# Performance work log

Hardware: AMD Instinct MI355X
Metric: run time of the kernel (lower is better)

## Reference

```python
import jax, jax.numpy as jnp
import numpy as np

MINC, MAXC, RATIO = 1, 16, 0.25


def _upsample2x(x):
    # bilinear, align_corners=False, (h,w) -> (2h,2w)
    B, C, h, w = x.shape
    def idx(n_in, n_out):
        src = (jnp.arange(n_out) + 0.5) * (n_in / n_out) - 0.5
        i0f = jnp.floor(src)
        t = (src - i0f).astype(jnp.float32)
        i0 = jnp.clip(i0f, 0, n_in - 1).astype(jnp.int32)
        i1 = jnp.clip(i0f + 1, 0, n_in - 1).astype(jnp.int32)
        return i0, i1, t
    i0, i1, t = idx(h, 2 * h)
    x = x[:, :, i0, :] * (1 - t)[None, None, :, None] + x[:, :, i1, :] * t[None, None, :, None]
    j0, j1, s = idx(w, 2 * w)
    x = x[:, :, :, j0] * (1 - s)[None, None, None, :] + x[:, :, :, j1] * s[None, None, None, :]
    return x


def _connection_counts(x):
    # DFDetector: down(0.5 bilinear, no antialias) == 2x2 avg-pool for even H,W
    B, C, H, W = x.shape
    xd = x.reshape(B, C, H // 2, 2, W // 2, 2).mean(axis=(3, 5))
    xu = _upsample2x(xd)
    df = jnp.abs(x - xu).sum(axis=1)  # [B,H,W]
    dmin = df.reshape(B, -1).min(axis=1)[:, None, None]
    dmax = df.reshape(B, -1).max(axis=1)[:, None, None]
    dn = (df - dmin) / (dmax - dmin + 1e-8)
    return (MINC + jnp.round(dn * (MAXC - MINC))).astype(jnp.int32)  # [B,H,W]


def setup_inputs() -> dict:
    key = jax.random.key(0)
    k0, k1, k2 = jax.random.split(key, 3)
    C = 64
    return {
        "x": jax.random.normal(k0, (2, C, 64, 64), jnp.float32),
        "ln_gamma": jnp.ones((C,), jnp.float32),
        "ln_beta": jnp.zeros((C,), jnp.float32),
        "w1": jax.random.normal(k1, (2 * C, C), jnp.float32) * 0.05,
        "b1": jnp.zeros((2 * C,), jnp.float32),
        "w2": jax.random.normal(k2, (C, 2 * C), jnp.float32) * 0.05,
        "b2": jnp.zeros((C,), jnp.float32),
    }


def reference(x, ln_gamma, ln_beta, w1, b1, w2, b2):
    B, C, H, W = x.shape
    k = _connection_counts(x).reshape(B, H * W)  # [B,HW] in [1,16]

    win = max(3, int(min(H, W) * RATIO))
    win += (win % 2 == 0)  # 17 for 64x64
    half = win // 2
    offs = np.arange(-half, half + 1)
    dy = np.repeat(offs, win); dx = np.tile(offs, win)             # [K2]
    py = np.repeat(np.arange(H), W); px = np.tile(np.arange(W), H)  # [HW]
    ny = py[:, None] + dy[None, :]; nx = px[:, None] + dx[None, :]
    valid = jnp.asarray((ny >= 0) & (ny < H) & (nx >= 0) & (nx < W))          # [HW,K2]
    idx = jnp.asarray(np.clip(ny, 0, H - 1) * W + np.clip(nx, 0, W - 1))      # [HW,K2]

    x_flat = x.transpose(0, 2, 3, 1).reshape(B, H * W, C)
    xn = x_flat / jnp.maximum(jnp.linalg.norm(x_flat, axis=-1, keepdims=True), 1e-12)

    nbr = xn[:, idx]                                   # [B,HW,K2,C]
    sim = jnp.einsum('bpc,bpkc->bpk', xn, nbr)         # cosine similarity
    sim = jnp.where(valid[None], sim, -1e30)           # mask out-of-bounds

    top_sim, top_i = jax.lax.top_k(sim, MAXC)          # [B,HW,16]
    mask = (jnp.arange(MAXC)[None, None, :] < k[:, :, None]).astype(x.dtype)
    wts = jnp.exp(top_sim) * mask
    wts = wts / wts.sum(-1, keepdims=True)

    gidx = jnp.take_along_axis(jnp.broadcast_to(idx[None], (B,) + idx.shape), top_i, axis=2)
    feats = jax.vmap(lambda xf, gi: xf[gi])(x_flat, gidx)  # [B,HW,16,C]
    agg = jnp.einsum('bpk,bpkc->bpc', wts, feats)
    out = agg.reshape(B, H, W, C).transpose(0, 3, 1, 2)

    # per-pixel channel LayerNorm (intent of nn.LayerNorm([C,1,1]))
    mu = x.mean(axis=1, keepdims=True)
    var = ((x - mu) ** 2).mean(axis=1, keepdims=True)
    xln = (x - mu) / jnp.sqrt(var + 1e-5) * ln_gamma[None, :, None, None] + ln_beta[None, :, None, None]

    enh = out + xln
    h1 = jax.nn.relu(jnp.einsum('bchw,dc->bdhw', enh, w1) + b1[None, :, None, None])
    ffn = jnp.einsum('bdhw,cd->bchw', h1, w2) + b2[None, :, None, None]
    return enh + ffn
```

## Files before the change

kernel.cpp:

```cpp
#include <hip/hip_runtime.h>
#include <math.h>

#define BB  2
#define CC  64
#define HH  64
#define WW  64
#define PP  4096
#define CHW 262144
#define KMAX 16
#define NSL 576

#define OFF_SIMS 0
#define OFF_XT   4718592
#define OFF_XNH  5242880
#define OFF_XNL  5505024
#define OFF_DF   5767168
#define OFF_PMN  5775360
#define OFF_PMX  5775616

typedef __bf16 bf16x8 __attribute__((ext_vector_type(8)));
typedef __bf16 bf16x4 __attribute__((ext_vector_type(4)));
typedef float  f32x4  __attribute__((ext_vector_type(4)));

#define DPP_STEP(v, ctrl, OP) { int _s = __builtin_amdgcn_update_dpp( \
    __float_as_int(v), __float_as_int(v), ctrl, 0xf, 0xf, false); \
    v = OP(v, __int_as_float(_s)); }
__device__ __forceinline__ float addf_(float a, float b) { return a + b; }
__device__ __forceinline__ float wave_max_b(float v) {
    DPP_STEP(v, 0x111, fmaxf) DPP_STEP(v, 0x112, fmaxf) DPP_STEP(v, 0x114, fmaxf)
    DPP_STEP(v, 0x118, fmaxf) DPP_STEP(v, 0x142, fmaxf) DPP_STEP(v, 0x143, fmaxf)
    return __int_as_float(__builtin_amdgcn_readlane(__float_as_int(v), 63));
}
__device__ __forceinline__ float wave_min_b(float v) {
    DPP_STEP(v, 0x111, fminf) DPP_STEP(v, 0x112, fminf) DPP_STEP(v, 0x114, fminf)
    DPP_STEP(v, 0x118, fminf) DPP_STEP(v, 0x142, fminf) DPP_STEP(v, 0x143, fminf)
    return __int_as_float(__builtin_amdgcn_readlane(__float_as_int(v), 63));
}
__device__ __forceinline__ float wave_sum_b(float v) {
    DPP_STEP(v, 0x111, addf_) DPP_STEP(v, 0x112, addf_) DPP_STEP(v, 0x114, addf_)
    DPP_STEP(v, 0x118, addf_) DPP_STEP(v, 0x142, addf_) DPP_STEP(v, 0x143, addf_)
    return __int_as_float(__builtin_amdgcn_readlane(__float_as_int(v), 63));
}

__global__ __launch_bounds__(256) void k_prep(const float* __restrict__ x,
        float* __restrict__ xt,
        unsigned short* __restrict__ xnh, unsigned short* __restrict__ xnl,
        float* __restrict__ df, float* __restrict__ pmn, float* __restrict__ pmx) {
    __shared__ float T[64*33];
    __shared__ float xds[2304];
    __shared__ float pdf[8*33], pss[8*33];
    __shared__ float sinv[32];
    int t = threadIdx.x;
    int bp0 = blockIdx.x * 32;
    int b = bp0 >> 12, p0 = bp0 & 4095;
    int y = p0 >> 6, x0 = p0 & 63;
    const float* xb = x + b*CHW + p0;
    #pragma unroll
    for (int i = 0; i < 8; ++i) {
        int idx = t + i*256;
        int c = idx >> 5, pxl = idx & 31;
        T[c*33 + pxl] = xb[c*PP + pxl];
    }
    int m = y >> 1;
    int R0, R1; float ty;
    if ((y & 1) == 0) { R0 = m > 0 ? m-1 : 0; R1 = m; ty = 0.75f; }
    else              { R0 = m; R1 = m < 31 ? m+1 : 31; ty = 0.25f; }
    int h0 = x0 >> 1;
    #pragma unroll
    for (int i = 0; i < 9; ++i) {
        int id = t + i*256;
        int c = id / 36, rem = id - c*36;
        int rr = (rem >= 18) ? 1 : 0, cc = rem - rr*18;
        int row = rr ? R1 : R0;
        int col = h0 - 1 + cc; col = col < 0 ? 0 : (col > 31 ? 31 : col);
        const float* xp = x + b*CHW + c*PP + row*2*WW + col*2;
        xds[id] = (xp[0] + xp[1] + xp[WW] + xp[WW+1]) * 0.25f;
    }
    __syncthreads();
    int px = t & 31, sl = t >> 5;
    int xxp = x0 + px;
    int n2 = xxp >> 1, jx0, jx1; float tx;
    if ((xxp & 1) == 0) { jx0 = n2 > 0 ? n2-1 : 0; jx1 = n2; tx = 0.75f; }
    else                { jx0 = n2; jx1 = n2 < 31 ? n2+1 : 31; tx = 0.25f; }
    int cc0 = jx0 - h0 + 1, cc1 = jx1 - h0 + 1;
    float dfa = 0.f, ss = 0.f;
    #pragma unroll
    for (int ci = 0; ci < 8; ++ci) {
        int c = sl*8 + ci;
        const float* xc = &xds[c*36];
        float a00 = xc[cc0],      a10 = xc[18 + cc0];
        float a01 = xc[cc1],      a11 = xc[18 + cc1];
        float r0 = a00*(1.f-ty) + a10*ty;
        float r1 = a01*(1.f-ty) + a11*ty;
        float xu = r0*(1.f-tx) + r1*tx;
        float v = T[c*33 + px];
        dfa += fabsf(v - xu);
        ss  += v*v;
    }
    pdf[sl*33 + px] = dfa; pss[sl*33 + px] = ss;
    __syncthreads();
    if (t < 32) {
        float d = 0.f, s = 0.f;
        #pragma unroll
        for (int q = 0; q < 8; ++q) { d += pdf[q*33 + t]; s += pss[q*33 + t]; }
        df[bp0 + t] = d;
        sinv[t] = 1.f / fmaxf(sqrtf(s), 1e-12f);
        float mn = d, mx = d;
        #pragma unroll
        for (int off = 1; off < 32; off <<= 1) {
            mn = fminf(mn, __shfl_xor(mn, off));
            mx = fmaxf(mx, __shfl_xor(mx, off));
        }
        if (t == 0) { pmn[blockIdx.x] = mn; pmx[blockIdx.x] = mx; }
    }
    __syncthreads();
    int px2 = t >> 3, cg = t & 7;
    float inv = sinv[px2];
    int bp = bp0 + px2;
    float4 f0, f1; bf16x8 hh, ll;
    #pragma unroll
    for (int k = 0; k < 8; ++k) {
        float v = T[(cg*8 + k)*33 + px2];
        if (k < 4) ((float*)&f0)[k] = v; else ((float*)&f1)[k-4] = v;
        float xnv = v * inv;
        __bf16 hb = (__bf16)xnv;
        float lo = xnv - (float)hb;
        hh[k] = hb; ll[k] = (__bf16)lo;
    }
    *(float4*)&xt[bp*64 + cg*8]     = f0;
    *(float4*)&xt[bp*64 + cg*8 + 4] = f1;
    *(bf16x8*)&xnh[bp*64 + cg*8] = hh;
    *(bf16x8*)&xnl[bp*64 + cg*8] = ll;
}

__global__ __launch_bounds__(256) void k_simA(
        const unsigned short* __restrict__ xnh,
        const unsigned short* __restrict__ xnl,
        float* __restrict__ simsT) {
    __shared__ unsigned short Ah[64*64], Al[64*64];
    __shared__ unsigned short Bh[64*64], Bl[64*64];
    int t = threadIdx.x;
    int bid = blockIdx.x;
    int tile = bid / 9, chunk = bid - tile*9;
    int b = tile >> 6, trow = (tile >> 3) & 7, tcol = tile & 7;
    int y0 = trow*8, x0 = tcol*8;
    int pbase = (b<<12) + y0*64 + x0;
    #pragma unroll
    for (int j = 0; j < 2; ++j) {
        int q = t + j*256;
        int row = q >> 3, kg = q & 7;
        int bp = pbase + ((row >> 3) << 6) + (row & 7);
        int src = bp*64 + kg*8;
        int dst = row*64 + ((kg ^ (row & 7)) << 3);
        *(bf16x8*)&Ah[dst] = *(const bf16x8*)&xnh[src];
        *(bf16x8*)&Al[dst] = *(const bf16x8*)&xnl[src];
    }
    #pragma unroll
    for (int j = 0; j < 2; ++j) {
        int q = t + j*256;
        int n = q >> 3, kg = q & 7;
        int S = chunk*64 + n;
        int r = S / 24, c = S - r*24;
        int ny = y0 + r - 8, nx = x0 + c - 8;
        bool vimg = (ny >= 0) && (ny < HH) && (nx >= 0) && (nx < WW);
        int dst = n*64 + ((kg ^ (n & 7)) << 3);
        if (vimg) {
            int bq = (b<<12) + ny*64 + nx;
            int src = bq*64 + kg*8;
            *(bf16x8*)&Bh[dst] = *(const bf16x8*)&xnh[src];
            *(bf16x8*)&Bl[dst] = *(const bf16x8*)&xnl[src];
        } else {
            bf16x8 z = {};
            *(bf16x8*)&Bh[dst] = z;
            *(bf16x8*)&Bl[dst] = z;
        }
    }
    __syncthreads();
    int w = t >> 6, l = t & 63;
    int lr = l & 15, lq = l >> 4;
    int nl = w*16 + lr;
    f32x4 acc[4];
    #pragma unroll
    for (int i = 0; i < 4; ++i) acc[i] = (f32x4){0.f,0.f,0.f,0.f};
    #pragma unroll
    for (int ks = 0; ks < 2; ++ks) {
        int bkg = ((ks*4 + lq) ^ (nl & 7)) << 3;
        bf16x8 bhi = *(bf16x8*)&Bh[nl*64 + bkg];
        bf16x8 blo = *(bf16x8*)&Bl[nl*64 + bkg];
        #pragma unroll
        for (int mt = 0; mt < 4; ++mt) {
            int arow = mt*16 + lr;
            int akg = ((ks*4 + lq) ^ (arow & 7)) << 3;
            bf16x8 ahi = *(bf16x8*)&Ah[arow*64 + akg];
            bf16x8 alo = *(bf16x8*)&Al[arow*64 + akg];
            acc[mt] = __builtin_amdgcn_mfma_f32_16x16x32_bf16(ahi, bhi, acc[mt], 0, 0, 0);
            acc[mt] = __builtin_amdgcn_mfma_f32_16x16x32_bf16(ahi, blo, acc[mt], 0, 0, 0);
            acc[mt] = __builtin_amdgcn_mfma_f32_16x16x32_bf16(alo, bhi, acc[mt], 0, 0, 0);
        }
    }
    int S = chunk*64 + nl;
    int r_slot = S / 24, c_slot = S - r_slot*24;
    int ny = y0 + r_slot - 8, nx = x0 + c_slot - 8;
    bool vimg = (ny >= 0) && (ny < HH) && (nx >= 0) && (nx < WW);
    float* tbase = simsT + (size_t)tile*64*NSL + chunk*64 + nl;
    #pragma unroll
    for (int mt = 0; mt < 4; ++mt) {
        #pragma unroll
        for (int r = 0; r < 4; ++r) {
            int px = mt*16 + lq*4 + r;
            tbase[(size_t)px*NSL] = vimg ? acc[mt][r] : -1e30f;
        }
    }
}

__global__ __launch_bounds__(1024) void k_simBF(const float* __restrict__ simsT,
        const float* __restrict__ xt, const float* __restrict__ df,
        const float* __restrict__ pmn, const float* __restrict__ pmx,
        const float* __restrict__ gamma, const float* __restrict__ beta,
        const float* __restrict__ w1, const float* __restrict__ b1,
        const float* __restrict__ w2, const float* __restrict__ b2,
        float* __restrict__ out) {
    __shared__ __bf16 w1bf[128*72];
    __shared__ __bf16 w2bf[64*136];
    __shared__ __bf16 enh16[16*72];
    __shared__ __bf16 h1bf[16*136];
    __shared__ float  enhT32[16*68];
    __shared__ float  smm[2];
    int t = threadIdx.x;
    int bp0 = blockIdx.x * 16;
    int b = bp0 >> 12;
    int pix0 = bp0 & 4095;
    #pragma unroll
    for (int j = 0; j < 2; ++j) {
        int i4 = t + j*1024;
        float4 v = *(const float4*)(w1 + i4*4);
        int dd = i4 >> 4, c0 = (i4 & 15)*4;
        bf16x4 h; h[0]=(__bf16)v.x; h[1]=(__bf16)v.y; h[2]=(__bf16)v.z; h[3]=(__bf16)v.w;
        *(bf16x4*)&w1bf[dd*72 + c0] = h;
    }
    #pragma unroll
    for (int j = 0; j < 2; ++j) {
        int i4 = t + j*1024;
        float4 v = *(const float4*)(w2 + i4*4);
        int cc2 = i4 >> 5, d0 = (i4 & 31)*4;
        bf16x4 h; h[0]=(__bf16)v.x; h[1]=(__bf16)v.y; h[2]=(__bf16)v.z; h[3]=(__bf16)v.w;
        *(bf16x4*)&w2bf[cc2*136 + d0] = h;
    }
    if (t < 64) {
        float v = fminf(pmn[b*128 + t], pmn[b*128 + 64 + t]);
        v = wave_min_b(v);
        if (t == 0) smm[0] = v;
    } else if (t < 128) {
        int u = t & 63;
        float v = fmaxf(pmx[b*128 + u], pmx[b*128 + 64 + u]);
        v = wave_max_b(v);
        if (u == 0) smm[1] = v;
    }
    __syncthreads();
    int wv = t >> 6, lane = t & 63;
    int bp = bp0 + wv;
    int p = bp & 4095, y = p >> 6, xx = p & 63;
    {
        int tile = (b << 6) + ((y >> 3) << 3) + (xx >> 3);
        int pxq = ((y & 7) << 3) + (xx & 7);
        int i_loc = y & 7, j_loc = xx & 7;
        const float* srow = simsT + ((size_t)tile*64 + pxq)*NSL;
        float tv[9];
        #pragma unroll
        for (int j = 0; j < 9; ++j) {
            int s = lane + (j << 6);
            int r = s / 24, c = s - r*24;
            int sy = r - i_loc, sx = c - j_loc;
            bool ok = ((unsigned)sy <= 16u) && ((unsigned)sx <= 16u);
            float v = srow[s];
            tv[j] = ok ? v : -1e30f;
        }
        float lbv = tv[0]; int lbj = 0;
        #pragma unroll
        for (int j = 1; j < 9; ++j) if (tv[j] > lbv) { lbv = tv[j]; lbj = j; }
        float dmin = smm[0], dmax = smm[1];
        float dn = (df[bp] - dmin) / (dmax - dmin + 1e-8f);
        int kk = 1 + (int)rintf(dn * 15.f);
        int y0 = y & ~7, x0 = xx & ~7;
        float S = 0.f, acc = 0.f;
        for (int rr = 0; rr < kk; ++rr) {
            float bv = wave_max_b(lbv);
            unsigned long long msk = __ballot(lbv == bv);
            int src = __ffsll(msk) - 1;
            int js = __builtin_amdgcn_readlane(lbj, src);
            int s = src + (js << 6);
            int r = s / 24, c = s - r*24;
            int ny = y0 + r - 8, nx = x0 + c - 8;
            int q = (b << 12) + ny*64 + nx;
            float e = expf(bv);
            S += e;
            acc += e * xt[q*64 + lane];
            if (lane == src) {
                #pragma unroll
                for (int j = 0; j < 9; ++j) if (j == lbj) tv[j] = -3e30f;
            }
            lbv = tv[0]; lbj = 0;
            #pragma unroll
            for (int j = 1; j < 9; ++j) if (tv[j] > lbv) { lbv = tv[j]; lbj = j; }
        }
        float xv = xt[bp*64 + lane];
        float mu = wave_sum_b(xv) * (1.f/64.f);
        float d = xv - mu;
        float var = wave_sum_b(d*d) * (1.f/64.f);
        float xln = d / sqrtf(var + 1e-5f) * gamma[lane] + beta[lane];
        float val = acc / S + xln;
        enhT32[wv*68 + lane] = val;
        enh16[wv*72 + lane] = (__bf16)val;
    }
    __syncthreads();
    int lr = lane & 15, lq = lane >> 4;
    if (wv < 8) {
        int d0 = wv*16;
        f32x4 acc1 = (f32x4){0.f,0.f,0.f,0.f};
        #pragma unroll
        for (int kh = 0; kh < 2; ++kh) {
            int kb = kh*32 + lq*8;
            bf16x8 a  = *(bf16x8*)&enh16[lr*72 + kb];
            bf16x8 bb = *(bf16x8*)&w1bf[(d0 + lr)*72 + kb];
            acc1 = __builtin_amdgcn_mfma_f32_16x16x32_bf16(a, bb, acc1, 0, 0, 0);
        }
        int dd = d0 + lr;
        float bias = b1[dd];
        #pragma unroll
        for (int r = 0; r < 4; ++r) {
            int pxr = lq*4 + r;
            h1bf[pxr*136 + dd] = (__bf16)fmaxf(acc1[r] + bias, 0.f);
        }
    }
    __syncthreads();
    if (wv < 4) {
        int c0 = wv*16;
        f32x4 acc2 = (f32x4){0.f,0.f,0.f,0.f};
        #pragma unroll
        for (int kh = 0; kh < 4; ++kh) {
            int kb = kh*32 + lq*8;
            bf16x8 a  = *(bf16x8*)&h1bf[lr*136 + kb];
            bf16x8 bb = *(bf16x8*)&w2bf[(c0 + lr)*136 + kb];
            acc2 = __builtin_amdgcn_mfma_f32_16x16x32_bf16(a, bb, acc2, 0, 0, 0);
        }
        int c = c0 + lr;
        float bias = b2[c];
        #pragma unroll
        for (int r = 0; r < 4; ++r) {
            int pxr = lq*4 + r;
            out[b*CHW + c*PP + pix0 + pxr] = acc2[r] + bias + enhT32[pxr*68 + c];
        }
    }
}

extern "C" void kernel_launch(void* const* d_in, const int* in_sizes, int n_in,
                              void* d_out, int out_size, void* d_ws, size_t ws_size,
                              hipStream_t stream) {
    const float* x     = (const float*)d_in[0];
    const float* gamma = (const float*)d_in[1];
    const float* beta  = (const float*)d_in[2];
    const float* w1    = (const float*)d_in[3];
    const float* b1    = (const float*)d_in[4];
    const float* w2    = (const float*)d_in[5];
    const float* b2    = (const float*)d_in[6];
    float* ws    = (float*)d_ws;
    float* simsT = ws + OFF_SIMS;
    float* xt    = ws + OFF_XT;
    float* df    = ws + OFF_DF;
    float* pmn   = ws + OFF_PMN;
    float* pmx   = ws + OFF_PMX;
    unsigned short* xnh = (unsigned short*)(ws + OFF_XNH);
    unsigned short* xnl = (unsigned short*)(ws + OFF_XNL);
    float* out   = (float*)d_out;

    k_prep<<<256, 256, 0, stream>>>(x, xt, xnh, xnl, df, pmn, pmx);
    k_simA<<<1152, 256, 0, stream>>>(xnh, xnl, simsT);
    k_simBF<<<512, 1024, 0, stream>>>(simsT, xt, df, pmn, pmx, gamma, beta,
                                      w1, b1, w2, b2, out);
}
```

Measured before the change: 39.35 us.

## Fuse similarity GEMM into top-k/FFN kernel with LDS-resident 4x8 tile sims

Merges the similarity-matrix kernel and the top-k/aggregation/FFN kernel into one kernel. Each block now handles a 4x8 pixel tile, computes its 480-slot neighbourhood similarities with MFMA directly into LDS, and then does top-k selection and the FFN from LDS. The goal is to drop the large global simsT round trip and one kernel launch. Weights are converted to bf16 into LDS space that is reused after the sims are consumed. The trade-offs are fewer blocks (256), MFMA operands loaded straight from global memory without LDS staging, and a smaller tile that raises the halo-to-output ratio.

```diff
diff --git a/kernel.cpp b/kernel.cpp
--- a/kernel.cpp
+++ b/kernel.cpp
@@ -8,15 +8,15 @@
 #define PP  4096
 #define CHW 262144
 #define KMAX 16
-#define NSL 576
-
-#define OFF_SIMS 0
-#define OFF_XT   4718592
-#define OFF_XNH  5242880
-#define OFF_XNL  5505024
-#define OFF_DF   5767168
-#define OFF_PMN  5775360
-#define OFF_PMX  5775616
+#define NSL 480
+#define SSTR 488
+
+#define OFF_XT   0
+#define OFF_XNH  524288
+#define OFF_XNL  786432
+#define OFF_DF   1048576
+#define OFF_PMN  1056768
+#define OFF_PMX  1057024
 
 typedef __bf16 bf16x8 __attribute__((ext_vector_type(8)));
 typedef __bf16 bf16x4 __attribute__((ext_vector_type(4)));
@@ -133,119 +133,32 @@
     *(bf16x8*)&xnl[bp*64 + cg*8] = ll;
 }
 
-__global__ __launch_bounds__(256) void k_simA(
+__global__ __launch_bounds__(512) void k_fused(
         const unsigned short* __restrict__ xnh,
         const unsigned short* __restrict__ xnl,
-        float* __restrict__ simsT) {
-    __shared__ unsigned short Ah[64*64], Al[64*64];
-    __shared__ unsigned short Bh[64*64], Bl[64*64];
-    int t = threadIdx.x;
-    int bid = blockIdx.x;
-    int tile = bid / 9, chunk = bid - tile*9;
-    int b = tile >> 6, trow = (tile >> 3) & 7, tcol = tile & 7;
-    int y0 = trow*8, x0 = tcol*8;
-    int pbase = (b<<12) + y0*64 + x0;
-    #pragma unroll
-    for (int j = 0; j < 2; ++j) {
-        int q = t + j*256;
-        int row = q >> 3, kg = q & 7;
-        int bp = pbase + ((row >> 3) << 6) + (row & 7);
-        int src = bp*64 + kg*8;
-        int dst = row*64 + ((kg ^ (row & 7)) << 3);
-        *(bf16x8*)&Ah[dst] = *(const bf16x8*)&xnh[src];
-        *(bf16x8*)&Al[dst] = *(const bf16x8*)&xnl[src];
-    }
-    #pragma unroll
-    for (int j = 0; j < 2; ++j) {
-        int q = t + j*256;
-        int n = q >> 3, kg = q & 7;
-        int S = chunk*64 + n;
-        int r = S / 24, c = S - r*24;
-        int ny = y0 + r - 8, nx = x0 + c - 8;
-        bool vimg = (ny >= 0) && (ny < HH) && (nx >= 0) && (nx < WW);
-        int dst = n*64 + ((kg ^ (n & 7)) << 3);
-        if (vimg) {
-            int bq = (b<<12) + ny*64 + nx;
-            int src = bq*64 + kg*8;
-            *(bf16x8*)&Bh[dst] = *(const bf16x8*)&xnh[src];
-            *(bf16x8*)&Bl[dst] = *(const bf16x8*)&xnl[src];
-        } else {
-            bf16x8 z = {};
-            *(bf16x8*)&Bh[dst] = z;
-            *(bf16x8*)&Bl[dst] = z;
-        }
-    }
-    __syncthreads();
-    int w = t >> 6, l = t & 63;
-    int lr = l & 15, lq = l >> 4;
-    int nl = w*16 + lr;
-    f32x4 acc[4];
-    #pragma unroll
-    for (int i = 0; i < 4; ++i) acc[i] = (f32x4){0.f,0.f,0.f,0.f};
-    #pragma unroll
-    for (int ks = 0; ks < 2; ++ks) {
-        int bkg = ((ks*4 + lq) ^ (nl & 7)) << 3;
-        bf16x8 bhi = *(bf16x8*)&Bh[nl*64 + bkg];
-        bf16x8 blo = *(bf16x8*)&Bl[nl*64 + bkg];
-        #pragma unroll
-        for (int mt = 0; mt < 4; ++mt) {
-            int arow = mt*16 + lr;
-            int akg = ((ks*4 + lq) ^ (arow & 7)) << 3;
-            bf16x8 ahi = *(bf16x8*)&Ah[arow*64 + akg];
-            bf16x8 alo = *(bf16x8*)&Al[arow*64 + akg];
-            acc[mt] = __builtin_amdgcn_mfma_f32_16x16x32_bf16(ahi, bhi, acc[mt], 0, 0, 0);
-            acc[mt] = __builtin_amdgcn_mfma_f32_16x16x32_bf16(ahi, blo, acc[mt], 0, 0, 0);
-            acc[mt] = __builtin_amdgcn_mfma_f32_16x16x32_bf16(alo, bhi, acc[mt], 0, 0, 0);
-        }
-    }
-    int S = chunk*64 + nl;
-    int r_slot = S / 24, c_slot = S - r_slot*24;
-    int ny = y0 + r_slot - 8, nx = x0 + c_slot - 8;
-    bool vimg = (ny >= 0) && (ny < HH) && (nx >= 0) && (nx < WW);
-    float* tbase = simsT + (size_t)tile*64*NSL + chunk*64 + nl;
-    #pragma unroll
-    for (int mt = 0; mt < 4; ++mt) {
-        #pragma unroll
-        for (int r = 0; r < 4; ++r) {
-            int px = mt*16 + lq*4 + r;
-            tbase[(size_t)px*NSL] = vimg ? acc[mt][r] : -1e30f;
-        }
-    }
-}
-
-__global__ __launch_bounds__(1024) void k_simBF(const float* __restrict__ simsT,
         const float* __restrict__ xt, const float* __restrict__ df,
         const float* __restrict__ pmn, const float* __restrict__ pmx,
         const float* __restrict__ gamma, const float* __restrict__ beta,
         const float* __restrict__ w1, const float* __restrict__ b1,
         const float* __restrict__ w2, const float* __restrict__ b2,
         float* __restrict__ out) {
-    __shared__ __bf16 w1bf[128*72];
-    __shared__ __bf16 w2bf[64*136];
-    __shared__ __bf16 enh16[16*72];
-    __shared__ __bf16 h1bf[16*136];
-    __shared__ float  enhT32[16*68];
+    __shared__ __align__(16) char U[32*SSTR*4];
+    float*  simsU = (float*)U;
+    __bf16* w1bf  = (__bf16*)U;
+    __bf16* w2bf  = (__bf16*)(U + 18432);
+    __bf16* h1bf  = (__bf16*)(U + 18432 + 17408);
+    __shared__ __bf16 enh16[32*72];
+    __shared__ float  enhT32[32*68];
     __shared__ float  smm[2];
     int t = threadIdx.x;
-    int bp0 = blockIdx.x * 16;
-    int b = bp0 >> 12;
-    int pix0 = bp0 & 4095;
-    #pragma unroll
-    for (int j = 0; j < 2; ++j) {
-        int i4 = t + j*1024;
-        float4 v = *(const float4*)(w1 + i4*4);
-        int dd = i4 >> 4, c0 = (i4 & 15)*4;
-        bf16x4 h; h[0]=(__bf16)v.x; h[1]=(__bf16)v.y; h[2]=(__bf16)v.z; h[3]=(__bf16)v.w;
-        *(bf16x4*)&w1bf[dd*72 + c0] = h;
-    }
-    #pragma unroll
-    for (int j = 0; j < 2; ++j) {
-        int i4 = t + j*1024;
-        float4 v = *(const float4*)(w2 + i4*4);
-        int cc2 = i4 >> 5, d0 = (i4 & 31)*4;
-        bf16x4 h; h[0]=(__bf16)v.x; h[1]=(__bf16)v.y; h[2]=(__bf16)v.z; h[3]=(__bf16)v.w;
-        *(bf16x4*)&w2bf[cc2*136 + d0] = h;
-    }
+    int bid = blockIdx.x;
+    int b = bid >> 7, tid = bid & 127;
+    int trow = tid >> 3, tcol = tid & 7;
+    int y0 = trow*4, x0 = tcol*8;
+    int pbase = (b << 12) + y0*64 + x0;
+    int pix0 = pbase & 4095;
+    int w = t >> 6, lane = t & 63;
+    int lr = lane & 15, lq = lane >> 4;
     if (t < 64) {
         float v = fminf(pmn[b*128 + t], pmn[b*128 + 64 + t]);
         v = wave_min_b(v);
@@ -256,32 +169,60 @@
         v = wave_max_b(v);
         if (u == 0) smm[1] = v;
     }
-    __syncthreads();
-    int wv = t >> 6, lane = t & 63;
-    int bp = bp0 + wv;
-    int p = bp & 4095, y = p >> 6, xx = p & 63;
     {
-        int tile = (b << 6) + ((y >> 3) << 3) + (xx >> 3);
-        int pxq = ((y & 7) << 3) + (xx & 7);
-        int i_loc = y & 7, j_loc = xx & 7;
-        const float* srow = simsT + ((size_t)tile*64 + pxq)*NSL;
-        float tv[9];
-        #pragma unroll
-        for (int j = 0; j < 9; ++j) {
+        int mt = w & 1, ng = w >> 1;
+        int pxA = mt*16 + lr;
+        int bpA = pbase + ((pxA >> 3) << 6) + (pxA & 7);
+        const unsigned short* ah = xnh + bpA*64 + lq*8;
+        const unsigned short* al = xnl + bpA*64 + lq*8;
+        bf16x8 ah0 = *(const bf16x8*)ah, ah1 = *(const bf16x8*)(ah + 32);
+        bf16x8 al0 = *(const bf16x8*)al, al1 = *(const bf16x8*)(al + 32);
+        for (int nt = ng; nt < 30; nt += 4) {
+            int S = nt*16 + lr;
+            int r = S / 24, c = S - r*24;
+            int ny = y0 + r - 8, nx = x0 + c - 8;
+            bool vimg = ((unsigned)ny < 64u) && ((unsigned)nx < 64u);
+            int bq = vimg ? (pbase + (r - 8)*64 + (c - 8)) : bpA;
+            const unsigned short* bh = xnh + bq*64 + lq*8;
+            const unsigned short* bl = xnl + bq*64 + lq*8;
+            bf16x8 bh0 = *(const bf16x8*)bh, bh1 = *(const bf16x8*)(bh + 32);
+            bf16x8 bl0 = *(const bf16x8*)bl, bl1 = *(const bf16x8*)(bl + 32);
+            f32x4 acc = (f32x4){0.f,0.f,0.f,0.f};
+            acc = __builtin_amdgcn_mfma_f32_16x16x32_bf16(ah0, bh0, acc, 0, 0, 0);
+            acc = __builtin_amdgcn_mfma_f32_16x16x32_bf16(ah0, bl0, acc, 0, 0, 0);
+            acc = __builtin_amdgcn_mfma_f32_16x16x32_bf16(al0, bh0, acc, 0, 0, 0);
+            acc = __builtin_amdgcn_mfma_f32_16x16x32_bf16(ah1, bh1, acc, 0, 0, 0);
+            acc = __builtin_amdgcn_mfma_f32_16x16x32_bf16(ah1, bl1, acc, 0, 0, 0);
+            acc = __builtin_amdgcn_mfma_f32_16x16x32_bf16(al1, bh1, acc, 0, 0, 0);
+            #pragma unroll
+            for (int rr = 0; rr < 4; ++rr) {
+                int pxo = mt*16 + lq*4 + rr;
+                simsU[pxo*SSTR + S] = vimg ? acc[rr] : -1e30f;
+            }
+        }
+    }
+    __syncthreads();
+    for (int ii = 0; ii < 4; ++ii) {
+        int px = w*4 + ii;
+        int i_loc = px >> 3, j_loc = px & 7;
+        int bp = pbase + i_loc*64 + j_loc;
+        const float* srow = simsU + px*SSTR;
+        float tv[8];
+        #pragma unroll
+        for (int j = 0; j < 8; ++j) {
             int s = lane + (j << 6);
+            bool in = (j < 7) || (lane < 32);
             int r = s / 24, c = s - r*24;
             int sy = r - i_loc, sx = c - j_loc;
-            bool ok = ((unsigned)sy <= 16u) && ((unsigned)sx <= 16u);
-            float v = srow[s];
-            tv[j] = ok ? v : -1e30f;
+            bool ok = in && ((unsigned)sy <= 16u) && ((unsigned)sx <= 16u);
+            tv[j] = ok ? srow[s] : -1e30f;
         }
         float lbv = tv[0]; int lbj = 0;
         #pragma unroll
-        for (int j = 1; j < 9; ++j) if (tv[j] > lbv) { lbv = tv[j]; lbj = j; }
+        for (int j = 1; j < 8; ++j) if (tv[j] > lbv) { lbv = tv[j]; lbj = j; }
         float dmin = smm[0], dmax = smm[1];
         float dn = (df[bp] - dmin) / (dmax - dmin + 1e-8f);
         int kk = 1 + (int)rintf(dn * 15.f);
-        int y0 = y & ~7, x0 = xx & ~7;
         float S = 0.f, acc = 0.f;
         for (int rr = 0; rr < kk; ++rr) {
             float bv = wave_max_b(lbv);
@@ -290,18 +231,17 @@
             int js = __builtin_amdgcn_readlane(lbj, src);
             int s = src + (js << 6);
             int r = s / 24, c = s - r*24;
-            int ny = y0 + r - 8, nx = x0 + c - 8;
-            int q = (b << 12) + ny*64 + nx;
+            int q = pbase + (r - 8)*64 + (c - 8);
             float e = expf(bv);
             S += e;
             acc += e * xt[q*64 + lane];
             if (lane == src) {
                 #pragma unroll
-                for (int j = 0; j < 9; ++j) if (j == lbj) tv[j] = -3e30f;
+                for (int j = 0; j < 8; ++j) if (j == lbj) tv[j] = -3e30f;
             }
             lbv = tv[0]; lbj = 0;
             #pragma unroll
-            for (int j = 1; j < 9; ++j) if (tv[j] > lbv) { lbv = tv[j]; lbj = j; }
+            for (int j = 1; j < 8; ++j) if (tv[j] > lbv) { lbv = tv[j]; lbj = j; }
         }
         float xv = xt[bp*64 + lane];
         float mu = wave_sum_b(xv) * (1.f/64.f);
@@ -309,37 +249,59 @@
         float var = wave_sum_b(d*d) * (1.f/64.f);
         float xln = d / sqrtf(var + 1e-5f) * gamma[lane] + beta[lane];
         float val = acc / S + xln;
-        enhT32[wv*68 + lane] = val;
-        enh16[wv*72 + lane] = (__bf16)val;
-    }
-    __syncthreads();
-    int lr = lane & 15, lq = lane >> 4;
-    if (wv < 8) {
-        int d0 = wv*16;
-        f32x4 acc1 = (f32x4){0.f,0.f,0.f,0.f};
-        #pragma unroll
-        for (int kh = 0; kh < 2; ++kh) {
-            int kb = kh*32 + lq*8;
-            bf16x8 a  = *(bf16x8*)&enh16[lr*72 + kb];
-            bf16x8 bb = *(bf16x8*)&w1bf[(d0 + lr)*72 + kb];
-            acc1 = __builtin_amdgcn_mfma_f32_16x16x32_bf16(a, bb, acc1, 0, 0, 0);
-        }
-        int dd = d0 + lr;
-        float bias = b1[dd];
-        #pragma unroll
-        for (int r = 0; r < 4; ++r) {
-            int pxr = lq*4 + r;
-            h1bf[pxr*136 + dd] = (__bf16)fmaxf(acc1[r] + bias, 0.f);
-        }
-    }
-    __syncthreads();
-    if (wv < 4) {
-        int c0 = wv*16;
+        enhT32[px*68 + lane] = val;
+        enh16[px*72 + lane] = (__bf16)val;
+    }
+    __syncthreads();
+    #pragma unroll
+    for (int j = 0; j < 4; ++j) {
+        int i4 = t + j*512;
+        float4 v = *(const float4*)(w1 + i4*4);
+        int dd = i4 >> 4, c0 = (i4 & 15)*4;
+        bf16x4 h; h[0]=(__bf16)v.x; h[1]=(__bf16)v.y; h[2]=(__bf16)v.z; h[3]=(__bf16)v.w;
+        *(bf16x4*)&w1bf[dd*72 + c0] = h;
+    }
+    #pragma unroll
+    for (int j = 0; j < 4; ++j) {
+        int i4 = t + j*512;
+        float4 v = *(const float4*)(w2 + i4*4);
+        int cc2 = i4 >> 5, d0 = (i4 & 31)*4;
+        bf16x4 h; h[0]=(__bf16)v.x; h[1]=(__bf16)v.y; h[2]=(__bf16)v.z; h[3]=(__bf16)v.w;
+        *(bf16x4*)&w2bf[cc2*136 + d0] = h;
+    }
+    __syncthreads();
+    {
+        int mt = w & 1;
+        #pragma unroll
+        for (int u = 0; u < 2; ++u) {
+            int ntile = (w >> 1)*2 + u;
+            int d0 = ntile*16;
+            f32x4 acc1 = (f32x4){0.f,0.f,0.f,0.f};
+            #pragma unroll
+            for (int kh = 0; kh < 2; ++kh) {
+                int kb = kh*32 + lq*8;
+                bf16x8 a  = *(bf16x8*)&enh16[(mt*16 + lr)*72 + kb];
+                bf16x8 bb = *(bf16x8*)&w1bf[(d0 + lr)*72 + kb];
+                acc1 = __builtin_amdgcn_mfma_f32_16x16x32_bf16(a, bb, acc1, 0, 0, 0);
+            }
+            int dd = d0 + lr;
+            float bias = b1[dd];
+            #pragma unroll
+            for (int r = 0; r < 4; ++r) {
+                int pxr = mt*16 + lq*4 + r;
+                h1bf[pxr*136 + dd] = (__bf16)fmaxf(acc1[r] + bias, 0.f);
+            }
+        }
+    }
+    __syncthreads();
+    {
+        int mt = w & 1, ct = w >> 1;
+        int c0 = ct*16;
         f32x4 acc2 = (f32x4){0.f,0.f,0.f,0.f};
         #pragma unroll
         for (int kh = 0; kh < 4; ++kh) {
             int kb = kh*32 + lq*8;
-            bf16x8 a  = *(bf16x8*)&h1bf[lr*136 + kb];
+            bf16x8 a  = *(bf16x8*)&h1bf[(mt*16 + lr)*136 + kb];
             bf16x8 bb = *(bf16x8*)&w2bf[(c0 + lr)*136 + kb];
             acc2 = __builtin_amdgcn_mfma_f32_16x16x32_bf16(a, bb, acc2, 0, 0, 0);
         }
@@ -347,8 +309,9 @@
         float bias = b2[c];
         #pragma unroll
         for (int r = 0; r < 4; ++r) {
-            int pxr = lq*4 + r;
-            out[b*CHW + c*PP + pix0 + pxr] = acc2[r] + bias + enhT32[pxr*68 + c];
+            int pxr = mt*16 + lq*4 + r;
+            int pix = pix0 + ((pxr >> 3) << 6) + (pxr & 7);
+            out[b*CHW + c*PP + pix] = acc2[r] + bias + enhT32[pxr*68 + c];
         }
     }
 }
@@ -363,18 +326,16 @@
     const float* b1    = (const float*)d_in[4];
     const float* w2    = (const float*)d_in[5];
     const float* b2    = (const float*)d_in[6];
-    float* ws    = (float*)d_ws;
-    float* simsT = ws + OFF_SIMS;
-    float* xt    = ws + OFF_XT;
-    float* df    = ws + OFF_DF;
-    float* pmn   = ws + OFF_PMN;
-    float* pmx   = ws + OFF_PMX;
+    float* ws  = (float*)d_ws;
+    float* xt  = ws + OFF_XT;
+    float* df  = ws + OFF_DF;
+    float* pmn = ws + OFF_PMN;
+    float* pmx = ws + OFF_PMX;
     unsigned short* xnh = (unsigned short*)(ws + OFF_XNH);
     unsigned short* xnl = (unsigned short*)(ws + OFF_XNL);
-    float* out   = (float*)d_out;
+    float* out = (float*)d_out;
 
     k_prep<<<256, 256, 0, stream>>>(x, xt, xnh, xnl, df, pmn, pmx);
-    k_simA<<<1152, 256, 0, stream>>>(xnh, xnl, simsT);
-    k_simBF<<<512, 1024, 0, stream>>>(simsT, xt, df, pmn, pmx, gamma, beta,
-                                      w1, b1, w2, b2, out);
-}
+    k_fused<<<256, 512, 0, stream>>>(xnh, xnl, xt, df, pmn, pmx, gamma, beta,
+                                     w1, b1, w2, b2, out);
+}
```

Result: slower. 45.96 us (+16.8%).

## Store only per-pixel 17x17 window similarities instead of full 24x24 tile slots

Applied to the files above, without the earlier changes.

The similarity buffer now holds, for each pixel, only its own 17x17 window (289 entries padded to 292) instead of the full 576-slot shared tile neighbourhood. The GEMM kernel scatters each result into the windows of the pixels that need it, and the top-k kernel reads 5 values per lane instead of 9, dropping the per-slot window-validity test. This roughly halves intermediate memory traffic and the register and compare work in the selection loop. In exchange the writes become scattered and uncoalesced, with a divergent bounds branch in the store.

```diff
diff --git a/kernel.cpp b/kernel.cpp
--- a/kernel.cpp
+++ b/kernel.cpp
@@ -8,15 +8,15 @@
 #define PP  4096
 #define CHW 262144
 #define KMAX 16
-#define NSL 576
+#define SIMP 292
 
 #define OFF_SIMS 0
-#define OFF_XT   4718592
-#define OFF_XNH  5242880
-#define OFF_XNL  5505024
-#define OFF_DF   5767168
-#define OFF_PMN  5775360
-#define OFF_PMX  5775616
+#define OFF_XT   2392064
+#define OFF_XNH  2916352
+#define OFF_XNL  3178496
+#define OFF_DF   3440640
+#define OFF_PMN  3448832
+#define OFF_PMX  3449088
 
 typedef __bf16 bf16x8 __attribute__((ext_vector_type(8)));
 typedef __bf16 bf16x4 __attribute__((ext_vector_type(4)));
@@ -136,7 +136,7 @@
 __global__ __launch_bounds__(256) void k_simA(
         const unsigned short* __restrict__ xnh,
         const unsigned short* __restrict__ xnl,
-        float* __restrict__ simsT) {
+        float* __restrict__ simsM) {
     __shared__ unsigned short Ah[64*64], Al[64*64];
     __shared__ unsigned short Bh[64*64], Bl[64*64];
     int t = threadIdx.x;
@@ -202,18 +202,22 @@
     int r_slot = S / 24, c_slot = S - r_slot*24;
     int ny = y0 + r_slot - 8, nx = x0 + c_slot - 8;
     bool vimg = (ny >= 0) && (ny < HH) && (nx >= 0) && (nx < WW);
-    float* tbase = simsT + (size_t)tile*64*NSL + chunk*64 + nl;
     #pragma unroll
     for (int mt = 0; mt < 4; ++mt) {
         #pragma unroll
         for (int r = 0; r < 4; ++r) {
             int px = mt*16 + lq*4 + r;
-            tbase[(size_t)px*NSL] = vimg ? acc[mt][r] : -1e30f;
-        }
-    }
-}
-
-__global__ __launch_bounds__(1024) void k_simBF(const float* __restrict__ simsT,
+            int i_loc = px >> 3, j_loc = px & 7;
+            int sy = r_slot - i_loc, sx = c_slot - j_loc;
+            if ((unsigned)sy <= 16u && (unsigned)sx <= 16u) {
+                int bp = pbase + i_loc*64 + j_loc;
+                simsM[bp*SIMP + sy*17 + sx] = vimg ? acc[mt][r] : -1e30f;
+            }
+        }
+    }
+}
+
+__global__ __launch_bounds__(1024) void k_simBF(const float* __restrict__ simsM,
         const float* __restrict__ xt, const float* __restrict__ df,
         const float* __restrict__ pmn, const float* __restrict__ pmx,
         const float* __restrict__ gamma, const float* __restrict__ beta,
@@ -261,27 +265,19 @@
     int bp = bp0 + wv;
     int p = bp & 4095, y = p >> 6, xx = p & 63;
     {
-        int tile = (b << 6) + ((y >> 3) << 3) + (xx >> 3);
-        int pxq = ((y & 7) << 3) + (xx & 7);
-        int i_loc = y & 7, j_loc = xx & 7;
-        const float* srow = simsT + ((size_t)tile*64 + pxq)*NSL;
-        float tv[9];
-        #pragma unroll
-        for (int j = 0; j < 9; ++j) {
-            int s = lane + (j << 6);
-            int r = s / 24, c = s - r*24;
-            int sy = r - i_loc, sx = c - j_loc;
-            bool ok = ((unsigned)sy <= 16u) && ((unsigned)sx <= 16u);
-            float v = srow[s];
-            tv[j] = ok ? v : -1e30f;
-        }
+        const float* srow = simsM + bp*SIMP;
+        float tv[5];
+        tv[0] = srow[lane];
+        tv[1] = srow[lane + 64];
+        tv[2] = srow[lane + 128];
+        tv[3] = srow[lane + 192];
+        tv[4] = (lane < 33) ? srow[lane + 256] : -1e30f;
         float lbv = tv[0]; int lbj = 0;
         #pragma unroll
-        for (int j = 1; j < 9; ++j) if (tv[j] > lbv) { lbv = tv[j]; lbj = j; }
+        for (int j = 1; j < 5; ++j) if (tv[j] > lbv) { lbv = tv[j]; lbj = j; }
         float dmin = smm[0], dmax = smm[1];
         float dn = (df[bp] - dmin) / (dmax - dmin + 1e-8f);
         int kk = 1 + (int)rintf(dn * 15.f);
-        int y0 = y & ~7, x0 = xx & ~7;
         float S = 0.f, acc = 0.f;
         for (int rr = 0; rr < kk; ++rr) {
             float bv = wave_max_b(lbv);
@@ -289,19 +285,19 @@
             int src = __ffsll(msk) - 1;
             int js = __builtin_amdgcn_readlane(lbj, src);
             int s = src + (js << 6);
-            int r = s / 24, c = s - r*24;
-            int ny = y0 + r - 8, nx = x0 + c - 8;
+            int a = s / 17;
+            int ny = y + a - 8, nx = xx + (s - a*17) - 8;
             int q = (b << 12) + ny*64 + nx;
             float e = expf(bv);
             S += e;
             acc += e * xt[q*64 + lane];
             if (lane == src) {
                 #pragma unroll
-                for (int j = 0; j < 9; ++j) if (j == lbj) tv[j] = -3e30f;
+                for (int j = 0; j < 5; ++j) if (j == lbj) tv[j] = -3e30f;
             }
             lbv = tv[0]; lbj = 0;
             #pragma unroll
-            for (int j = 1; j < 9; ++j) if (tv[j] > lbv) { lbv = tv[j]; lbj = j; }
+            for (int j = 1; j < 5; ++j) if (tv[j] > lbv) { lbv = tv[j]; lbj = j; }
         }
         float xv = xt[bp*64 + lane];
         float mu = wave_sum_b(xv) * (1.f/64.f);
@@ -364,7 +360,7 @@
     const float* w2    = (const float*)d_in[5];
     const float* b2    = (const float*)d_in[6];
     float* ws    = (float*)d_ws;
-    float* simsT = ws + OFF_SIMS;
+    float* simsM = ws + OFF_SIMS;
     float* xt    = ws + OFF_XT;
     float* df    = ws + OFF_DF;
     float* pmn   = ws + OFF_PMN;
@@ -374,7 +370,7 @@
     float* out   = (float*)d_out;
 
     k_prep<<<256, 256, 0, stream>>>(x, xt, xnh, xnl, df, pmn, pmx);
-    k_simA<<<1152, 256, 0, stream>>>(xnh, xnl, simsT);
-    k_simBF<<<512, 1024, 0, stream>>>(simsT, xt, df, pmn, pmx, gamma, beta,
+    k_simA<<<1152, 256, 0, stream>>>(xnh, xnl, simsM);
+    k_simBF<<<512, 1024, 0, stream>>>(simsM, xt, df, pmn, pmx, gamma, beta,
                                       w1, b1, w2, b2, out);
 }
```

New measurement: 37.41 us. 4.9% less time.
